# Kernel tuning notes

Hardware: AMD Instinct MI355X
Metric: run time of the kernel (lower is better)

Reference implementation:

```python
import jax, jax.numpy as jnp
import numpy as np

KS = 5   # kernel_size per pseudo-dim
DIM = 3  # pseudo-coordinate dim
S = 2 ** DIM  # contributing B-spline (degree 1) basis combos per edge


def spline_conv(x, edge_index, pseudo, weight, root, bias, kernel_size=KS, dim=DIM):
    """Degree-1 open B-spline conv (PyG SplineConv, aggr='mean', root_weight, bias)."""
    src, dst = edge_index[0], edge_index[1]
    N, Cin = x.shape
    Ktot, _, Cout = weight.shape  # Ktot = kernel_size**dim
    v = pseudo * (kernel_size - 1)          # open spline: [E, dim]
    lo = jnp.floor(v)
    frac = v - lo
    lo = lo.astype(jnp.int32)
    bits = ((jnp.arange(S)[:, None] >> jnp.arange(dim)[None, :]) & 1)  # [S, dim]
    b = jnp.where(bits[None] == 1, frac[:, None, :], 1.0 - frac[:, None, :])  # [E,S,dim]
    basis = jnp.prod(b, axis=-1)                                            # [E,S]
    idx = jnp.clip(lo[:, None, :] + bits[None], 0, kernel_size - 1)          # [E,S,dim]
    mult = (kernel_size ** jnp.arange(dim)).astype(jnp.int32)
    kidx = jnp.sum(idx * mult, axis=-1)                                      # [E,S]
    xj = x[src]                                                              # [E,Cin]
    contrib = (basis[:, :, None] * xj[:, None, :]).reshape(-1, Cin)          # [E*S,Cin]
    seg = (dst[:, None] * Ktot + kidx).reshape(-1)                           # [E*S]
    # A[n,k,i] = sum of basis-weighted source features per (target node, kernel idx)
    A = jax.ops.segment_sum(contrib, seg, num_segments=N * Ktot).reshape(N, Ktot, Cin)
    deg = jax.ops.segment_sum(jnp.ones_like(dst, jnp.float32), dst, num_segments=N)
    out = jnp.einsum('nki,kio->no', A, weight) / jnp.maximum(deg, 1.0)[:, None]
    return out + x @ root + bias


def knn_interp(x, pos_x, pos_y, batch_x, batch_y, k):
    # squared dists via gemm: [Ny, Nx]
    d2 = (jnp.sum(pos_y * pos_y, -1)[:, None]
          + jnp.sum(pos_x * pos_x, -1)[None, :]
          - 2.0 * pos_y @ pos_x.T)
    d2 = jnp.where(batch_y[:, None] != batch_x[None, :], 1e10, d2)
    neg, idx = jax.lax.top_k(-d2, k)                  # [Ny, k]
    w = 1.0 / jnp.maximum(-neg, 1e-16)                # inverse-squared-distance weights
    w = jax.lax.stop_gradient(w)                      # PyG computes weights under no_grad
    num = jnp.einsum('yk,ykc->yc', w, x[idx])
    return num / jnp.sum(w, -1, keepdims=True)


def setup_inputs() -> dict:
    key = jax.random.key(0)
    ks = jax.random.split(key, 8)
    Nx, Ny, E, Cin, Cout = 4096, 16384, 65536, 64, 64
    return {
        'x': jax.random.normal(ks[0], (Nx, Cin), jnp.float32),
        'pos_x': jax.random.normal(ks[1], (Nx, DIM), jnp.float32),
        'pos_y': jax.random.normal(ks[2], (Ny, DIM), jnp.float32),
        'edge_index': jax.random.randint(ks[3], (2, E), 0, Nx, jnp.int32),
        'edge_attr': jax.random.uniform(ks[4], (E, DIM), jnp.float32),
        'batch_x': jnp.zeros((Nx,), jnp.int32),
        'batch_y': jnp.zeros((Ny,), jnp.int32),
        'weight': jax.random.normal(ks[5], (KS ** DIM, Cin, Cout), jnp.float32) * 0.05,
        'root': jax.random.normal(ks[6], (Cin, Cout), jnp.float32) * 0.05,
        'bias': jnp.zeros((Cout,), jnp.float32),
        'k': 3,
    }


def reference(x, pos_x, pos_y, edge_index, edge_attr, batch_x, batch_y, weight, root, bias, k):
    h = jax.nn.elu(spline_conv(x, edge_index, edge_attr, weight, root, bias))
    return knn_interp(h, pos_x, pos_y, batch_x, batch_y, k)
```

## Files before the change

### kernel.cpp

```cpp
#include <hip/hip_runtime.h>
#include <stdint.h>

#define WAVE 64
#define CIN 64
#define COUT 64
#define KS 5
#define KTOT 125
#define NSPLIT 16
#define BM 1e5f

typedef __attribute__((ext_vector_type(8))) short short8v;
typedef __attribute__((ext_vector_type(4))) float f32x4;

__device__ inline unsigned long long wmin64(unsigned long long v) {
#pragma unroll
  for (int o = 32; o >= 1; o >>= 1) {
    unsigned long long u = __shfl_xor(v, o, 64);
    v = (u < v) ? u : v;
  }
  return v;
}

__device__ inline unsigned f32_orderable(float f) {
  unsigned fb = __float_as_uint(f);
  return (fb & 0x80000000u) ? ~fb : (fb | 0x80000000u);
}
__device__ inline float f32_unorderable(unsigned u) {
  unsigned fb = (u & 0x80000000u) ? (u & 0x7fffffffu) : ~u;
  return __uint_as_float(fb);
}

__device__ inline unsigned short f2bf(float f) {
  unsigned u = __float_as_uint(f);
  unsigned r = (u + 0x7fffu + ((u >> 16) & 1u)) >> 16;
  return (unsigned short)r;
}
__device__ inline float bf2f(unsigned short v) {
  return __uint_as_float(((unsigned)v) << 16);
}

__device__ __forceinline__ float qnorm4(float q0, float q1, float q2, float q3) {
  return fmaf(q0, q0, fmaf(q1, q1, fmaf(q2, q2, q3 * q3)));
}
__device__ __forceinline__ float dist2(float q0, float q1, float q2, float q3,
                                       float py2t, float4 c, float c3) {
  float dot = fmaf(q0, c.x, fmaf(q1, c.y, fmaf(q2, c.z, q3 * c3)));
  return fmaf(-2.f, dot, py2t + c.w);
}

__device__ inline void edge_basis(const float* __restrict__ pseudo, int e,
                                  float bas[8], int kidx[8]) {
  float v0 = pseudo[e * 3 + 0] * (float)(KS - 1);
  float v1 = pseudo[e * 3 + 1] * (float)(KS - 1);
  float v2 = pseudo[e * 3 + 2] * (float)(KS - 1);
  float l0 = floorf(v0), l1 = floorf(v1), l2 = floorf(v2);
  float f0 = v0 - l0, f1 = v1 - l1, f2 = v2 - l2;
  int i0 = (int)l0, i1 = (int)l1, i2 = (int)l2;
#pragma unroll
  for (int s = 0; s < 8; s++) {
    int b0 = s & 1, b1 = (s >> 1) & 1, b2 = (s >> 2) & 1;
    float bb = (b0 ? f0 : 1.f - f0) * (b1 ? f1 : 1.f - f1) * (b2 ? f2 : 1.f - f2);
    int j0 = i0 + b0; j0 = j0 < 0 ? 0 : (j0 > KS - 1 ? KS - 1 : j0);
    int j1 = i1 + b1; j1 = j1 < 0 ? 0 : (j1 > KS - 1 ? KS - 1 : j1);
    int j2 = i2 + b2; j2 = j2 < 0 ? 0 : (j2 > KS - 1 ? KS - 1 : j2);
    bas[s] = bb;
    kidx[s] = j0 + KS * j1 + KS * KS * j2;
  }
}

__global__ __launch_bounds__(256) void pre_kernel(
    const float* __restrict__ x, unsigned short* __restrict__ xbf, int n4,
    const float* __restrict__ Wf, unsigned short* __restrict__ wbf,
    const float* __restrict__ pos_x, const int* __restrict__ batch_x,
    float4* __restrict__ pxp4, float* __restrict__ pxb, int Nx_,
    int nb_cvtx) {
  __shared__ float L[64][68];
  int bid = blockIdx.x;
  int tid = threadIdx.x;

  if (bid < nb_cvtx) {
    int i = bid * 256 + tid;
    if (i >= n4) return;
    float4 v = *(const float4*)&x[i * 4];
    *(ushort4*)&xbf[i * 4] =
        make_ushort4(f2bf(v.x), f2bf(v.y), f2bf(v.z), f2bf(v.w));
    return;
  }
  bid -= nb_cvtx;
  if (bid < KTOT) {
    int k = bid;
    {
      int i = tid >> 2, o0 = (tid & 3) * 16;
      const float* src = Wf + (size_t)k * 4096 + i * 64 + o0;
      float4 a = *(const float4*)src;
      float4 b = *(const float4*)(src + 4);
      float4 c = *(const float4*)(src + 8);
      float4 d = *(const float4*)(src + 12);
      *(float4*)&L[i][o0 + 0] = a;
      *(float4*)&L[i][o0 + 4] = b;
      *(float4*)&L[i][o0 + 8] = c;
      *(float4*)&L[i][o0 + 12] = d;
    }
    __syncthreads();
    int o = tid >> 2, i0 = (tid & 3) * 16;
    unsigned short* dst = wbf + (size_t)k * 4096 + o * 64 + i0;
#pragma unroll
    for (int g = 0; g < 4; g++) {
      *(ushort4*)&dst[g * 4] =
          make_ushort4(f2bf(L[i0 + g * 4 + 0][o]), f2bf(L[i0 + g * 4 + 1][o]),
                       f2bf(L[i0 + g * 4 + 2][o]), f2bf(L[i0 + g * 4 + 3][o]));
    }
    return;
  }
  bid -= KTOT;
  {
    int t = bid * 256 + tid;
    if (t >= Nx_) return;
    float a0 = pos_x[t * 3 + 0], a1 = pos_x[t * 3 + 1], a2 = pos_x[t * 3 + 2];
    float bm = (float)batch_x[t] * BM;
    pxp4[t] = make_float4(a0, a1, a2, qnorm4(a0, a1, a2, bm));
    pxb[t] = bm;
  }
}

__global__ __launch_bounds__(256) void phaseQ_kernel(
    const float4* __restrict__ pxp4, const float* __restrict__ pxb,
    const float* __restrict__ pos_y, const int* __restrict__ batch_y,
    const int* __restrict__ kptr, float* __restrict__ vpart,
    int Ny_, int csize, int nb_knn, int nqb,
    const unsigned short* __restrict__ xbf,
    const unsigned short* __restrict__ wbf,
    unsigned short* __restrict__ xw, int Nx_, int nxb) {
  __shared__ char smem[8192];
  int bid = blockIdx.x;
  int tid = threadIdx.x;

  if (bid < nb_knn) {
    if (*kptr > 3) return;
    float4* lc = (float4*)smem;
    float* lb = (float*)(smem + 4096);
    const float FINF = __uint_as_float(0x7f800000u);

    int split = bid / nqb;
    int qy = (bid % nqb) * 256 + tid;
    int base0 = split * csize;

    int qc = qy < Ny_ ? qy : Ny_ - 1;
    float q0 = pos_y[qc * 3 + 0], q1 = pos_y[qc * 3 + 1], q2 = pos_y[qc * 3 + 2];
    float q3 = (float)batch_y[qc] * BM;
    float py2t = qnorm4(q0, q1, q2, q3);

    float b0 = FINF, b1 = FINF, b2 = FINF;

    for (int tb = 0; tb < csize; tb += 256) {
      int t = base0 + tb + tid;
      float4 cv;
      float cb;
      if (t < Nx_) {
        cv = pxp4[t];
        cb = pxb[t];
      } else {
        cv = make_float4(0.f, 0.f, 0.f, FINF);
        cb = 0.f;
      }
      __syncthreads();
      lc[tid] = cv;
      lb[tid] = cb;
      __syncthreads();

#pragma unroll 4
      for (int j = 0; j < 256; j++) {
        float d2 = dist2(q0, q1, q2, q3, py2t, lc[j], lb[j]);
        float n0 = fminf(d2, b0);
        float n1 = fminf(fmaxf(d2, b0), b1);
        float n2 = fminf(fmaxf(d2, b1), b2);
        b0 = n0; b1 = n1; b2 = n2;
      }
    }

    if (qy < Ny_) {
      float* vp = vpart + ((size_t)split * Ny_ + qy) * 3;
      vp[0] = b0;
      vp[1] = b1;
      vp[2] = b2;
    }
    return;
  }

  {
    int b = bid - nb_knn;
    int n0 = (b % nxb) * 64;
    int k = b / nxb;
    unsigned short(*S)[64] = (unsigned short(*)[64])smem;

    int w = tid >> 6, lane = tid & 63;
    int lr = lane & 15, kg = lane >> 4;
    int rA = n0 + w * 16 + lr;
    if (rA >= Nx_) rA = Nx_ - 1;

    short8v a0 = *(const short8v*)&xbf[(size_t)rA * CIN + kg * 8];
    short8v a1 = *(const short8v*)&xbf[(size_t)rA * CIN + 32 + kg * 8];

    const unsigned short* wb = wbf + (size_t)k * 4096;
#pragma unroll
    for (int ct = 0; ct < 4; ct++) {
      int col = ct * 16 + lr;
      short8v b0 = *(const short8v*)&wb[col * 64 + kg * 8];
      short8v b1 = *(const short8v*)&wb[col * 64 + 32 + kg * 8];
      f32x4 c = {0.f, 0.f, 0.f, 0.f};
      c = __builtin_amdgcn_mfma_f32_16x16x32_bf16(a0, b0, c, 0, 0, 0);
      c = __builtin_amdgcn_mfma_f32_16x16x32_bf16(a1, b1, c, 0, 0, 0);
#pragma unroll
      for (int r = 0; r < 4; r++) {
        S[w * 16 + kg * 4 + r][ct * 16 + lr] = f2bf(c[r]);
      }
    }
    __syncthreads();

#pragma unroll
    for (int round = 0; round < 2; round++) {
      int rr = (tid >> 3) + round * 32;
      int ch = (tid & 7) * 8;
      int grow = n0 + rr;
      if (grow < Nx_) {
        uint4 v = *(const uint4*)&S[rr][ch];
        *(uint4*)&xw[((size_t)k * Nx_ + grow) * COUT + ch] = v;
      }
    }
  }
}

__global__ __launch_bounds__(256) void phaseR_kernel(
    const float* __restrict__ vpart,
    const float4* __restrict__ pxp4, const float* __restrict__ pxb,
    const float* __restrict__ pos_y, const int* __restrict__ batch_y,
    const int* __restrict__ kptr, unsigned long long* __restrict__ part,
    int Ny_, int csize, int nb_knn, int nqb,
    const int* __restrict__ ei, const float* __restrict__ pseudo,
    const unsigned short* __restrict__ xw, float* __restrict__ acc,
    float* __restrict__ deg, int E_, int Nx_) {
  __shared__ char smem[5120];
  int bid = blockIdx.x;
  int tid = threadIdx.x;

  if (bid < nb_knn) {
    int kk = *kptr;
    if (kk > 3) return;
    kk = kk < 1 ? 1 : kk;
    float4* lc = (float4*)smem;
    float* lb = (float*)(smem + 4096);
    const float FINF = __uint_as_float(0x7f800000u);

    int split = bid / nqb;
    int qy = (bid % nqb) * 256 + tid;
    int base0 = split * csize;

    int qc = qy < Ny_ ? qy : Ny_ - 1;
    float q0 = pos_y[qc * 3 + 0], q1 = pos_y[qc * 3 + 1], q2 = pos_y[qc * 3 + 2];
    float q3 = (float)batch_y[qc] * BM;
    float py2t = qnorm4(q0, q1, q2, q3);

    float t0v = FINF, t1v = FINF, t2v = FINF;
#pragma unroll
    for (int s = 0; s < NSPLIT; s++) {
      const float* vp = vpart + ((size_t)s * Ny_ + qc) * 3;
#pragma unroll
      for (int r = 0; r < 3; r++) {
        float v = vp[r];
        float n0 = fminf(v, t0v);
        float n1 = fminf(fmaxf(v, t0v), t1v);
        float n2 = fminf(fmaxf(v, t1v), t2v);
        t0v = n0; t1v = n1; t2v = n2;
      }
    }
    float thr = kk == 1 ? t0v : (kk == 2 ? t1v : t2v);

    unsigned long long k0 = ~0ull, k1 = ~0ull, k2 = ~0ull;

    for (int tb = 0; tb < csize; tb += 256) {
      int t = base0 + tb + tid;
      float4 cv;
      float cb;
      if (t < Nx_) {
        cv = pxp4[t];
        cb = pxb[t];
      } else {
        cv = make_float4(0.f, 0.f, 0.f, FINF);
        cb = 0.f;
      }
      __syncthreads();
      lc[tid] = cv;
      lb[tid] = cb;
      __syncthreads();

#pragma unroll 4
      for (int j = 0; j < 256; j++) {
        float d2 = dist2(q0, q1, q2, q3, py2t, lc[j], lb[j]);
        if (d2 <= thr) {
          unsigned long long key =
              (((unsigned long long)f32_orderable(d2)) << 32) |
              (unsigned)(base0 + tb + j);
          {
            bool lt = key < k0;
            unsigned long long nv = lt ? key : k0;
            unsigned long long xv = lt ? k0 : key;
            k0 = nv; key = xv;
          }
          {
            bool lt = key < k1;
            unsigned long long nv = lt ? key : k1;
            unsigned long long xv = lt ? k1 : key;
            k1 = nv; key = xv;
          }
          k2 = key < k2 ? key : k2;
        }
      }
    }

    if (qy < Ny_) {
      unsigned long long* pp = part + ((size_t)split * Ny_ + qy) * 3;
      pp[0] = k0;
      pp[1] = k1;
      pp[2] = k2;
    }
    return;
  }

  {
    int b = bid - nb_knn;
    int lane = tid & 63;
    int e = (int)(((size_t)b * 256 + tid) >> 6);
    if (e >= E_) return;
    int src = ei[e];
    int dst = ei[E_ + e];
    float bas[8];
    int kidx[8];
    edge_basis(pseudo, e, bas, kidx);

    float y = 0.f;
#pragma unroll
    for (int s = 0; s < 8; s++) {
      y = fmaf(bas[s], bf2f(xw[((size_t)kidx[s] * Nx_ + src) * COUT + lane]), y);
    }
    atomicAdd(&acc[(size_t)dst * COUT + lane], y);
    if (lane == 0) atomicAdd(&deg[dst], 1.f);
  }
}

__global__ void node_finish_kernel(const float* __restrict__ x,
                                   const float* __restrict__ root,
                                   const float* __restrict__ bias,
                                   const float* __restrict__ acc,
                                   const float* __restrict__ deg,
                                   float* __restrict__ h, int Nx_) {
  int lane = threadIdx.x & 63;
  int n = (int)((blockIdx.x * blockDim.x + threadIdx.x) >> 6);
  if (n >= Nx_) return;
  float xs = x[(size_t)n * CIN + lane];
  float r = 0.f;
#pragma unroll 4
  for (int i = 0; i < CIN; i++) {
    float xv = __shfl(xs, i, 64);
    r = fmaf(xv, root[i * COUT + lane], r);
  }
  float d = deg[n];
  d = d > 1.f ? d : 1.f;
  float o = acc[(size_t)n * COUT + lane] / d + r + bias[lane];
  h[(size_t)n * COUT + lane] = (o > 0.f) ? o : expm1f(o);
}

__global__ void knn_merge_kernel(const unsigned long long* __restrict__ part,
                                 const float* __restrict__ h,
                                 const int* __restrict__ kptr,
                                 float* __restrict__ out, int Nx_, int Ny_) {
  int kk = *kptr;
  if (kk > 3) return;
  kk = kk < 1 ? 1 : kk;
  int lane = threadIdx.x & 63;
  int qy = (int)((blockIdx.x * blockDim.x + threadIdx.x) >> 6);
  if (qy >= Ny_) return;

  unsigned long long key = ~0ull;
  if (lane < 3 * NSPLIT) {
    key = part[((size_t)(lane / 3) * Ny_ + qy) * 3 + (lane % 3)];
  }

  float num = 0.f, den = 0.f;
  for (int i = 0; i < kk; i++) {
    unsigned long long m = wmin64(key);
    if (key == m) key = ~0ull;
    unsigned u = (unsigned)(m >> 32);
    int idx = (int)(m & 0xffffffffu);
    idx = (idx < 0 || idx >= Nx_) ? 0 : idx;
    float d2 = f32_unorderable(u);
    float w = 1.f / fmaxf(d2, 1e-16f);
    num = fmaf(w, h[(size_t)idx * COUT + lane], num);
    den += w;
  }
  out[(size_t)qy * COUT + lane] = num / den;
}

__global__ void knn_generic_kernel(const float* __restrict__ h,
                                   const float4* __restrict__ pxp4,
                                   const float* __restrict__ pxb,
                                   const float* __restrict__ pos_y,
                                   const int* __restrict__ batch_y,
                                   const int* __restrict__ kptr,
                                   float* __restrict__ out,
                                   int Nx_, int Ny_) {
  int kk = *kptr;
  if (kk <= 3) return;
  kk = kk > 8 ? 8 : kk;
  int lane = threadIdx.x & 63;
  int yy = (int)((blockIdx.x * blockDim.x + threadIdx.x) >> 6);
  if (yy >= Ny_) return;

  float q0 = pos_y[yy * 3 + 0], q1 = pos_y[yy * 3 + 1], q2 = pos_y[yy * 3 + 2];
  float q3 = (float)batch_y[yy] * BM;
  float py2t = qnorm4(q0, q1, q2, q3);

  unsigned long long best[8];
#pragma unroll
  for (int j = 0; j < 8; j++) best[j] = ~0ull;

  for (int t0 = 0; t0 < Nx_; t0 += 64) {
    int t = t0 + lane;
    unsigned long long key = ~0ull;
    if (t < Nx_) {
      float d2 = dist2(q0, q1, q2, q3, py2t, pxp4[t], pxb[t]);
      key = (((unsigned long long)f32_orderable(d2)) << 32) | (unsigned)t;
    }
    if (key < best[7]) {
#pragma unroll
      for (int j = 0; j < 8; j++) {
        unsigned long long mn = key < best[j] ? key : best[j];
        unsigned long long mx = key < best[j] ? best[j] : key;
        best[j] = mn;
        key = mx;
      }
    }
  }

  float num = 0.f, den = 0.f;
  for (int j = 0; j < kk; j++) {
    unsigned long long m = wmin64(best[0]);
    if (best[0] == m) {
#pragma unroll
      for (int t = 0; t < 7; t++) best[t] = best[t + 1];
      best[7] = ~0ull;
    }
    unsigned u = (unsigned)(m >> 32);
    int idx = (int)(m & 0xffffffffu);
    idx = (idx < 0 || idx >= Nx_) ? 0 : idx;
    float d2 = f32_unorderable(u);
    float w = 1.f / fmaxf(d2, 1e-16f);
    num = fmaf(w, h[(size_t)idx * COUT + lane], num);
    den += w;
  }
  out[(size_t)yy * COUT + lane] = num / den;
}

extern "C" void kernel_launch(void* const* d_in, const int* in_sizes, int n_in,
                              void* d_out, int out_size, void* d_ws, size_t ws_size,
                              hipStream_t stream) {
  const float* x = (const float*)d_in[0];
  const float* pos_x = (const float*)d_in[1];
  const float* pos_y = (const float*)d_in[2];
  const int* eidx = (const int*)d_in[3];
  const float* pseudo = (const float*)d_in[4];
  const int* batch_x = (const int*)d_in[5];
  const int* batch_y = (const int*)d_in[6];
  const float* W = (const float*)d_in[7];
  const float* root = (const float*)d_in[8];
  const float* bias = (const float*)d_in[9];
  const int* kptr = (const int*)d_in[10];

  int Nx = in_sizes[0] / CIN;
  int Ny = in_sizes[2] / 3;
  int E = in_sizes[3] / 2;

  int csize = ((Nx + NSPLIT - 1) / NSPLIT + 255) & ~255;
  if (csize < 256) csize = 256;

  float* acc = (float*)d_ws;
  float* deg = acc + (size_t)Nx * COUT;
  float* h = deg + Nx;
  float4* pxp4 = (float4*)(h + (size_t)Nx * COUT);
  float* pxb = (float*)(pxp4 + Nx);
  unsigned short* xbf = (unsigned short*)(pxb + Nx);
  unsigned short* wbf = xbf + (size_t)Nx * CIN;
  unsigned short* xw = wbf + (size_t)KTOT * CIN * COUT;
  float* vpart = (float*)(xw + (size_t)Nx * KTOT * COUT);
  uintptr_t paddr = (uintptr_t)(vpart + (size_t)NSPLIT * Ny * 3);
  paddr = (paddr + 7) & ~(uintptr_t)7;
  unsigned long long* part = (unsigned long long*)paddr;

  float* out = (float*)d_out;

  hipMemsetAsync(acc, 0, ((size_t)Nx * COUT + Nx) * sizeof(float), stream);

  int n4 = Nx * CIN / 4;
  int nb_cvtx = (n4 + 255) / 256;
  int nb_pack = (Nx + 255) / 256;
  int nqb = (Ny + 255) / 256;
  int nb_knn = nqb * NSPLIT;
  int nxb = (Nx + 63) / 64;
  int nb_edge = ((size_t)E * WAVE + 255) / 256;

  pre_kernel<<<nb_cvtx + KTOT + nb_pack, 256, 0, stream>>>(
      x, xbf, n4, W, wbf, pos_x, batch_x, pxp4, pxb, Nx, nb_cvtx);

  phaseQ_kernel<<<nb_knn + nxb * KTOT, 256, 0, stream>>>(
      pxp4, pxb, pos_y, batch_y, kptr, vpart, Ny, csize, nb_knn, nqb,
      xbf, wbf, xw, Nx, nxb);

  phaseR_kernel<<<nb_knn + nb_edge, 256, 0, stream>>>(
      vpart, pxp4, pxb, pos_y, batch_y, kptr, part, Ny, csize, nb_knn, nqb,
      eidx, pseudo, xw, acc, deg, E, Nx);

  {
    int blocks = (Nx * WAVE + 255) / 256;
    node_finish_kernel<<<blocks, 256, 0, stream>>>(x, root, bias, acc, deg, h, Nx);
  }
  {
    int blocks = (Ny * WAVE + 255) / 256;
    knn_merge_kernel<<<blocks, 256, 0, stream>>>(part, h, kptr, out, Nx, Ny);
    knn_generic_kernel<<<blocks, 256, 0, stream>>>(h, pxp4, pxb, pos_y, batch_y,
                                                   kptr, out, Nx, Ny);
  }
}
```

Baseline: 108.5 us.

## Interleave knn blocks among GEMM/edge blocks and fold memset into pre kernel

Spreads the long-running knn blocks evenly through the grid, one every S blocks, instead of putting them all first in phaseQ and phaseR. The intent is to balance heavy and light blocks across CUs so the knn work overlaps with the xw GEMM and edge scatter work instead of clustering. The hipMemsetAsync of the accumulators is also replaced by zeroing blocks inside pre_kernel, removing a separate memset launch. The trade-off is extra index arithmetic per block and a dependence on the block scheduler's dispatch order.

```diff
diff --git a/kernel.cpp b/kernel.cpp
--- a/kernel.cpp
+++ b/kernel.cpp
@@ -73,11 +73,17 @@
     const float* __restrict__ Wf, unsigned short* __restrict__ wbf,
     const float* __restrict__ pos_x, const int* __restrict__ batch_x,
     float4* __restrict__ pxp4, float* __restrict__ pxb, int Nx_,
-    int nb_cvtx) {
+    float* __restrict__ zbase, int nz4, int nb_zero, int nb_cvtx) {
   __shared__ float L[64][68];
   int bid = blockIdx.x;
   int tid = threadIdx.x;
 
+  if (bid < nb_zero) {
+    int i = bid * 256 + tid;
+    if (i < nz4) *(float4*)&zbase[i * 4] = make_float4(0.f, 0.f, 0.f, 0.f);
+    return;
+  }
+  bid -= nb_zero;
   if (bid < nb_cvtx) {
     int i = bid * 256 + tid;
     if (i >= n4) return;
@@ -127,7 +133,7 @@
     const float4* __restrict__ pxp4, const float* __restrict__ pxb,
     const float* __restrict__ pos_y, const int* __restrict__ batch_y,
     const int* __restrict__ kptr, float* __restrict__ vpart,
-    int Ny_, int csize, int nb_knn, int nqb,
+    int Ny_, int csize, int nb_knn, int nqb, int S,
     const unsigned short* __restrict__ xbf,
     const unsigned short* __restrict__ wbf,
     unsigned short* __restrict__ xw, int Nx_, int nxb) {
@@ -135,14 +141,17 @@
   int bid = blockIdx.x;
   int tid = threadIdx.x;
 
-  if (bid < nb_knn) {
+  int strip = bid / S;
+  bool isKnn = (bid % S == 0) && (strip < nb_knn);
+
+  if (isKnn) {
     if (*kptr > 3) return;
     float4* lc = (float4*)smem;
     float* lb = (float*)(smem + 4096);
     const float FINF = __uint_as_float(0x7f800000u);
 
-    int split = bid / nqb;
-    int qy = (bid % nqb) * 256 + tid;
+    int split = strip / nqb;
+    int qy = (strip % nqb) * 256 + tid;
     int base0 = split * csize;
 
     int qc = qy < Ny_ ? qy : Ny_ - 1;
@@ -188,10 +197,12 @@
   }
 
   {
-    int b = bid - nb_knn;
+    int nknn_below = (bid + S - 1) / S;
+    if (nknn_below > nb_knn) nknn_below = nb_knn;
+    int b = bid - nknn_below;
     int n0 = (b % nxb) * 64;
     int k = b / nxb;
-    unsigned short(*S)[64] = (unsigned short(*)[64])smem;
+    unsigned short(*Sm)[64] = (unsigned short(*)[64])smem;
 
     int w = tid >> 6, lane = tid & 63;
     int lr = lane & 15, kg = lane >> 4;
@@ -212,7 +223,7 @@
       c = __builtin_amdgcn_mfma_f32_16x16x32_bf16(a1, b1, c, 0, 0, 0);
 #pragma unroll
       for (int r = 0; r < 4; r++) {
-        S[w * 16 + kg * 4 + r][ct * 16 + lr] = f2bf(c[r]);
+        Sm[w * 16 + kg * 4 + r][ct * 16 + lr] = f2bf(c[r]);
       }
     }
     __syncthreads();
@@ -223,7 +234,7 @@
       int ch = (tid & 7) * 8;
       int grow = n0 + rr;
       if (grow < Nx_) {
-        uint4 v = *(const uint4*)&S[rr][ch];
+        uint4 v = *(const uint4*)&Sm[rr][ch];
         *(uint4*)&xw[((size_t)k * Nx_ + grow) * COUT + ch] = v;
       }
     }
@@ -235,7 +246,7 @@
     const float4* __restrict__ pxp4, const float* __restrict__ pxb,
     const float* __restrict__ pos_y, const int* __restrict__ batch_y,
     const int* __restrict__ kptr, unsigned long long* __restrict__ part,
-    int Ny_, int csize, int nb_knn, int nqb,
+    int Ny_, int csize, int nb_knn, int nqb, int S,
     const int* __restrict__ ei, const float* __restrict__ pseudo,
     const unsigned short* __restrict__ xw, float* __restrict__ acc,
     float* __restrict__ deg, int E_, int Nx_) {
@@ -243,7 +254,10 @@
   int bid = blockIdx.x;
   int tid = threadIdx.x;
 
-  if (bid < nb_knn) {
+  int strip = bid / S;
+  bool isKnn = (bid % S == 0) && (strip < nb_knn);
+
+  if (isKnn) {
     int kk = *kptr;
     if (kk > 3) return;
     kk = kk < 1 ? 1 : kk;
@@ -251,8 +265,8 @@
     float* lb = (float*)(smem + 4096);
     const float FINF = __uint_as_float(0x7f800000u);
 
-    int split = bid / nqb;
-    int qy = (bid % nqb) * 256 + tid;
+    int split = strip / nqb;
+    int qy = (strip % nqb) * 256 + tid;
     int base0 = split * csize;
 
     int qc = qy < Ny_ ? qy : Ny_ - 1;
@@ -327,7 +341,9 @@
   }
 
   {
-    int b = bid - nb_knn;
+    int nknn_below = (bid + S - 1) / S;
+    if (nknn_below > nb_knn) nknn_below = nb_knn;
+    int b = bid - nknn_below;
     int lane = tid & 63;
     int e = (int)(((size_t)b * 256 + tid) >> 6);
     if (e >= E_) return;
@@ -497,26 +513,38 @@
 
   float* out = (float*)d_out;
 
-  hipMemsetAsync(acc, 0, ((size_t)Nx * COUT + Nx) * sizeof(float), stream);
-
   int n4 = Nx * CIN / 4;
   int nb_cvtx = (n4 + 255) / 256;
   int nb_pack = (Nx + 255) / 256;
+  int nz4 = (Nx * COUT + Nx) / 4;
+  int nb_zero = (nz4 + 255) / 256;
   int nqb = (Ny + 255) / 256;
   int nb_knn = nqb * NSPLIT;
   int nxb = (Nx + 63) / 64;
-  int nb_edge = ((size_t)E * WAVE + 255) / 256;
-
-  pre_kernel<<<nb_cvtx + KTOT + nb_pack, 256, 0, stream>>>(
-      x, xbf, n4, W, wbf, pos_x, batch_x, pxp4, pxb, Nx, nb_cvtx);
-
-  phaseQ_kernel<<<nb_knn + nxb * KTOT, 256, 0, stream>>>(
-      pxp4, pxb, pos_y, batch_y, kptr, vpart, Ny, csize, nb_knn, nqb,
-      xbf, wbf, xw, Nx, nxb);
-
-  phaseR_kernel<<<nb_knn + nb_edge, 256, 0, stream>>>(
-      vpart, pxp4, pxb, pos_y, batch_y, kptr, part, Ny, csize, nb_knn, nqb,
-      eidx, pseudo, xw, acc, deg, E, Nx);
+  int nb_xw = nxb * KTOT;
+  int nb_edge = (int)(((size_t)E * WAVE + 255) / 256);
+
+  pre_kernel<<<nb_zero + nb_cvtx + KTOT + nb_pack, 256, 0, stream>>>(
+      x, xbf, n4, W, wbf, pos_x, batch_x, pxp4, pxb, Nx, acc, nz4, nb_zero,
+      nb_cvtx);
+
+  {
+    int total = nb_knn + nb_xw;
+    int S = total / nb_knn;
+    if (S < 1) S = 1;
+    phaseQ_kernel<<<total, 256, 0, stream>>>(
+        pxp4, pxb, pos_y, batch_y, kptr, vpart, Ny, csize, nb_knn, nqb, S,
+        xbf, wbf, xw, Nx, nxb);
+  }
+
+  {
+    int total = nb_knn + nb_edge;
+    int S = total / nb_knn;
+    if (S < 1) S = 1;
+    phaseR_kernel<<<total, 256, 0, stream>>>(
+        vpart, pxp4, pxb, pos_y, batch_y, kptr, part, Ny, csize, nb_knn, nqb, S,
+        eidx, pseudo, xw, acc, deg, E, Nx);
+  }
 
   {
     int blocks = (Nx * WAVE + 255) / 256;
```

New measurement: 187.0 us. 1.72x slower.

## Fold accumulator zeroing into pre kernel and batch four kernel taps per xw block

Applied to the files above, without the earlier changes.

Removes the separate hipMemsetAsync by adding zeroing blocks to pre_kernel, which saves one launch or memset node. In phaseQ, each xw block now computes four kernel taps instead of one and reuses the A fragments it already loaded, so there are about four times fewer blocks. Each loop iteration adds an extra __syncthreads, and the lower block count may reduce overlap with the knn blocks that share the launch.

```diff
diff --git a/kernel.cpp b/kernel.cpp
--- a/kernel.cpp
+++ b/kernel.cpp
@@ -7,6 +7,7 @@
 #define KS 5
 #define KTOT 125
 #define NSPLIT 16
+#define KB4 32
 #define BM 1e5f
 
 typedef __attribute__((ext_vector_type(8))) short short8v;
@@ -73,11 +74,17 @@
     const float* __restrict__ Wf, unsigned short* __restrict__ wbf,
     const float* __restrict__ pos_x, const int* __restrict__ batch_x,
     float4* __restrict__ pxp4, float* __restrict__ pxb, int Nx_,
-    int nb_cvtx) {
+    float* __restrict__ zbase, int nz4, int nb_zero, int nb_cvtx) {
   __shared__ float L[64][68];
   int bid = blockIdx.x;
   int tid = threadIdx.x;
 
+  if (bid < nb_zero) {
+    int i = bid * 256 + tid;
+    if (i < nz4) *(float4*)&zbase[i * 4] = make_float4(0.f, 0.f, 0.f, 0.f);
+    return;
+  }
+  bid -= nb_zero;
   if (bid < nb_cvtx) {
     int i = bid * 256 + tid;
     if (i >= n4) return;
@@ -190,8 +197,8 @@
   {
     int b = bid - nb_knn;
     int n0 = (b % nxb) * 64;
-    int k = b / nxb;
-    unsigned short(*S)[64] = (unsigned short(*)[64])smem;
+    int kg4 = b / nxb;
+    unsigned short(*Sm)[64] = (unsigned short(*)[64])smem;
 
     int w = tid >> 6, lane = tid & 63;
     int lr = lane & 15, kg = lane >> 4;
@@ -201,31 +208,36 @@
     short8v a0 = *(const short8v*)&xbf[(size_t)rA * CIN + kg * 8];
     short8v a1 = *(const short8v*)&xbf[(size_t)rA * CIN + 32 + kg * 8];
 
-    const unsigned short* wb = wbf + (size_t)k * 4096;
-#pragma unroll
-    for (int ct = 0; ct < 4; ct++) {
-      int col = ct * 16 + lr;
-      short8v b0 = *(const short8v*)&wb[col * 64 + kg * 8];
-      short8v b1 = *(const short8v*)&wb[col * 64 + 32 + kg * 8];
-      f32x4 c = {0.f, 0.f, 0.f, 0.f};
-      c = __builtin_amdgcn_mfma_f32_16x16x32_bf16(a0, b0, c, 0, 0, 0);
-      c = __builtin_amdgcn_mfma_f32_16x16x32_bf16(a1, b1, c, 0, 0, 0);
-#pragma unroll
-      for (int r = 0; r < 4; r++) {
-        S[w * 16 + kg * 4 + r][ct * 16 + lr] = f2bf(c[r]);
-      }
-    }
-    __syncthreads();
-
-#pragma unroll
-    for (int round = 0; round < 2; round++) {
-      int rr = (tid >> 3) + round * 32;
-      int ch = (tid & 7) * 8;
-      int grow = n0 + rr;
-      if (grow < Nx_) {
-        uint4 v = *(const uint4*)&S[rr][ch];
-        *(uint4*)&xw[((size_t)k * Nx_ + grow) * COUT + ch] = v;
-      }
+    for (int kk4 = 0; kk4 < 4; kk4++) {
+      int k = kg4 * 4 + kk4;
+      if (k >= KTOT) break;
+      const unsigned short* wb = wbf + (size_t)k * 4096;
+#pragma unroll
+      for (int ct = 0; ct < 4; ct++) {
+        int col = ct * 16 + lr;
+        short8v b0 = *(const short8v*)&wb[col * 64 + kg * 8];
+        short8v b1 = *(const short8v*)&wb[col * 64 + 32 + kg * 8];
+        f32x4 c = {0.f, 0.f, 0.f, 0.f};
+        c = __builtin_amdgcn_mfma_f32_16x16x32_bf16(a0, b0, c, 0, 0, 0);
+        c = __builtin_amdgcn_mfma_f32_16x16x32_bf16(a1, b1, c, 0, 0, 0);
+#pragma unroll
+        for (int r = 0; r < 4; r++) {
+          Sm[w * 16 + kg * 4 + r][ct * 16 + lr] = f2bf(c[r]);
+        }
+      }
+      __syncthreads();
+
+#pragma unroll
+      for (int round = 0; round < 2; round++) {
+        int rr = (tid >> 3) + round * 32;
+        int ch = (tid & 7) * 8;
+        int grow = n0 + rr;
+        if (grow < Nx_) {
+          uint4 v = *(const uint4*)&Sm[rr][ch];
+          *(uint4*)&xw[((size_t)k * Nx_ + grow) * COUT + ch] = v;
+        }
+      }
+      __syncthreads();
     }
   }
 }
@@ -497,20 +509,23 @@
 
   float* out = (float*)d_out;
 
-  hipMemsetAsync(acc, 0, ((size_t)Nx * COUT + Nx) * sizeof(float), stream);
-
   int n4 = Nx * CIN / 4;
   int nb_cvtx = (n4 + 255) / 256;
   int nb_pack = (Nx + 255) / 256;
+  int nz4 = (Nx * COUT + Nx) / 4;
+  int nb_zero = (nz4 + 255) / 256;
   int nqb = (Ny + 255) / 256;
   int nb_knn = nqb * NSPLIT;
   int nxb = (Nx + 63) / 64;
-  int nb_edge = ((size_t)E * WAVE + 255) / 256;
-
-  pre_kernel<<<nb_cvtx + KTOT + nb_pack, 256, 0, stream>>>(
-      x, xbf, n4, W, wbf, pos_x, batch_x, pxp4, pxb, Nx, nb_cvtx);
-
-  phaseQ_kernel<<<nb_knn + nxb * KTOT, 256, 0, stream>>>(
+  int nkg4 = (KTOT + 3) / 4;
+  int nb_xw = nxb * nkg4;
+  int nb_edge = (int)(((size_t)E * WAVE + 255) / 256);
+
+  pre_kernel<<<nb_zero + nb_cvtx + KTOT + nb_pack, 256, 0, stream>>>(
+      x, xbf, n4, W, wbf, pos_x, batch_x, pxp4, pxb, Nx, acc, nz4, nb_zero,
+      nb_cvtx);
+
+  phaseQ_kernel<<<nb_knn + nb_xw, 256, 0, stream>>>(
       pxp4, pxb, pos_y, batch_y, kptr, vpart, Ny, csize, nb_knn, nqb,
       xbf, wbf, xw, Nx, nxb);
 
```

After: 102.9 us. 5.2% less time.
